# Optimization experiments

Hardware: AMD Instinct MI355X
Metric: run time of the kernel (lower is better)

## Reference

```python
import jax, jax.numpy as jnp
import numpy as np

GROUPS = 32
EPS = 1e-5
NUM_HEADS = 8


def group_norm(x, w, b):
    # x: (B, C, H, W)
    B, C, H, W = x.shape
    xg = x.reshape(B, GROUPS, C // GROUPS, H, W)
    mean = xg.mean(axis=(2, 3, 4), keepdims=True)
    var = xg.var(axis=(2, 3, 4), keepdims=True)
    xg = (xg - mean) * jax.lax.rsqrt(var + EPS)
    x = xg.reshape(B, C, H, W)
    return x * w[None, :, None, None] + b[None, :, None, None]


def setup_inputs() -> dict:
    key = jax.random.key(0)
    ks = jax.random.split(key, 4)
    B, C, H, W = 16, 512, 32, 32
    x = jax.random.normal(ks[0], (B, C, H, W), dtype=jnp.float32)
    gn_w = jnp.ones((C,), dtype=jnp.float32)
    gn_b = jnp.zeros((C,), dtype=jnp.float32)
    qkv_w = jax.random.normal(ks[1], (3 * C, C), dtype=jnp.float32) * 0.02  # 1x1 conv, no bias
    proj_w = jax.random.normal(ks[2], (C, C), dtype=jnp.float32) * 0.02     # 1x1 conv
    proj_b = jax.random.normal(ks[3], (C,), dtype=jnp.float32) * 0.02
    return {"x": x, "gn_w": gn_w, "gn_b": gn_b, "qkv_w": qkv_w,
            "proj_w": proj_w, "proj_b": proj_b}


def reference(x, gn_w, gn_b, qkv_w, proj_w, proj_b):
    B, C, H, W = x.shape
    heads = NUM_HEADS
    head_dim = C // heads
    HW = H * W
    scale = 1.0 / (head_dim ** 0.5)

    x = group_norm(x, gn_w, gn_b)  # residual uses the NORMED x, matching source

    qkv = jnp.einsum('bchw,oc->bohw', x, qkv_w)                     # (B, 3C, H, W)
    qkv = qkv.reshape(B, 3, heads, head_dim, HW)
    q, k, v = qkv[:, 0], qkv[:, 1], qkv[:, 2]                       # (B, heads, head_dim, HW)

    # Replicate the source's exact permute(0,2,3,1)+reshape (scrambles semantics, but faithful)
    def to_bmh(t):
        return jnp.transpose(t, (0, 2, 3, 1)).reshape(B * heads, HW, head_dim)
    q, k, v = to_bmh(q), to_bmh(k), to_bmh(v)

    attn = jax.nn.softmax(jnp.einsum('bnd,bmd->bnm', q, k) * scale, axis=-1)  # (B*heads, HW, HW)
    h = jnp.einsum('bnm,bmd->bnd', attn, v)                                   # (B*heads, HW, head_dim)

    h = h.reshape(B, heads, H, W, head_dim)
    h = jnp.transpose(h, (0, 1, 4, 2, 3)).reshape(B, C, H, W)

    out = jnp.einsum('bchw,oc->bohw', h, proj_w) + proj_b[None, :, None, None]
    return out + x
```

## Files before the change

### kernel.cpp

```cpp
#include <hip/hip_runtime.h>
#include <stdint.h>

typedef unsigned short u16;
typedef short bfrag __attribute__((ext_vector_type(8)));
typedef float ffrag __attribute__((ext_vector_type(4)));
typedef u16 us4 __attribute__((ext_vector_type(4)));
typedef uint32_t u32x4 __attribute__((ext_vector_type(4)));

#define HW 1024
#define C_DIM 512
#define O3 1536
#define BATCH 16

__device__ __forceinline__ u16 f2bf(float f) {
    uint32_t u = __builtin_bit_cast(uint32_t, f);
    u += 0x7FFFu + ((u >> 16) & 1u);
    return (u16)(u >> 16);
}
__device__ __forceinline__ float bf2f(u16 v) {
    return __builtin_bit_cast(float, (uint32_t)v << 16);
}
__device__ __forceinline__ float fexp2(float x) { return __builtin_amdgcn_exp2f(x); }
__device__ __forceinline__ void async16(const u16* src, u16* ldsDst) {
    __builtin_amdgcn_global_load_lds(
        (const __attribute__((address_space(1))) uint32_t*)src,
        (__attribute__((address_space(3))) uint32_t*)ldsDst, 16, 0, 0);
}

__global__ __launch_bounds__(256) void cvt2_kernel(const float* __restrict__ a, u16* __restrict__ da, int n4a,
                                                   const float* __restrict__ b, u16* __restrict__ db, int n4b) {
    int i = blockIdx.x * 256 + threadIdx.x;
    if (i < n4a) {
        float4 v = ((const float4*)a)[i];
        us4 o = { f2bf(v.x), f2bf(v.y), f2bf(v.z), f2bf(v.w) };
        ((us4*)da)[i] = o;
    } else {
        int j = i - n4a;
        if (j < n4b) {
            float4 v = ((const float4*)b)[j];
            us4 o = { f2bf(v.x), f2bf(v.y), f2bf(v.z), f2bf(v.w) };
            ((us4*)db)[j] = o;
        }
    }
}

__global__ __launch_bounds__(256) void groupnorm_kernel(
    const float* __restrict__ x, const float* __restrict__ gw, const float* __restrict__ gb,
    u16* __restrict__ xg, u16* __restrict__ xgt)
{
    __shared__ u16 tile[16 * 1032];
    __shared__ float red[8];
    const int tid = threadIdx.x;
    const int batch = blockIdx.x >> 5, g = blockIdx.x & 31;
    const float* xp = x + ((size_t)batch * C_DIM + g * 16) * HW;

    float s = 0.f, ss = 0.f;
#pragma unroll
    for (int it = 0; it < 16; ++it) {
        int i4 = it * 256 + tid;
        float4 v = ((const float4*)xp)[i4];
        int ci = i4 >> 8;
        int hw = (i4 & 255) * 4;
        s += v.x + v.y + v.z + v.w;
        ss += v.x * v.x + v.y * v.y + v.z * v.z + v.w * v.w;
        us4 u = { f2bf(v.x), f2bf(v.y), f2bf(v.z), f2bf(v.w) };
        *(us4*)&tile[ci * 1032 + hw] = u;
    }
#pragma unroll
    for (int m = 1; m <= 32; m <<= 1) { s += __shfl_xor(s, m, 64); ss += __shfl_xor(ss, m, 64); }
    if ((tid & 63) == 0) { red[tid >> 6] = s; red[4 + (tid >> 6)] = ss; }
    __syncthreads();
    float S = red[0] + red[1] + red[2] + red[3];
    float SS = red[4] + red[5] + red[6] + red[7];
    const float mean = S * (1.f / 16384.f);
    const float istd = rsqrtf(SS * (1.f / 16384.f) - mean * mean + 1e-5f);

    u16* xgp = xg + ((size_t)batch * C_DIM + g * 16) * HW;
#pragma unroll
    for (int it = 0; it < 16; ++it) {
        int i4 = it * 256 + tid;
        int ci = i4 >> 8;
        int hw = (i4 & 255) * 4;
        us4 u = *(us4*)&tile[ci * 1032 + hw];
        float sc = gw[g * 16 + ci] * istd;
        float bi = gb[g * 16 + ci] - mean * sc;
        us4 o = { f2bf(bf2f(u[0]) * sc + bi), f2bf(bf2f(u[1]) * sc + bi),
                  f2bf(bf2f(u[2]) * sc + bi), f2bf(bf2f(u[3]) * sc + bi) };
        *(us4*)&xgp[(size_t)ci * HW + hw] = o;
    }
    u16* xtp = xgt + (size_t)batch * HW * C_DIM + g * 16;
#pragma unroll
    for (int it = 0; it < 16; ++it) {
        int hw = (tid >> 2) + it * 64;
        int c0 = (tid & 3) * 4;
        us4 o;
#pragma unroll
        for (int k2 = 0; k2 < 4; ++k2) {
            int ci = c0 + k2;
            float sc = gw[g * 16 + ci] * istd;
            float bi = gb[g * 16 + ci] - mean * sc;
            o[k2] = f2bf(bf2f(tile[ci * 1032 + hw]) * sc + bi);
        }
        *(us4*)&xtp[(size_t)hw * C_DIM + c0] = o;
    }
}

__global__ __launch_bounds__(256, 2) void qkv_gemm_kernel(
    const u16* __restrict__ A, const u16* __restrict__ B, u16* __restrict__ Out,
    u16* __restrict__ vtout)
{
    __shared__ __align__(16) u16 smem[36864];
    const int tid = threadIdx.x;
    const int l = tid & 63, w = tid >> 6;
    const int swz = (blockIdx.x & 7) * 96 + (blockIdx.x >> 3);
    const int batch = swz / 48, t = swz % 48;
    const int tm = t / 12, tn = t % 12;
    A += (size_t)batch * (HW * C_DIM) + (size_t)tm * 256 * 512;
    B += (size_t)tn * 128 * 512;

    auto stageA = [&](u16* lds, int kt) {
#pragma unroll
        for (int i = 0; i < 4; ++i) {
            int L = i * 256 + tid;
            int row = L >> 2, cs = L & 3;
            int c = cs ^ ((row & 3) ^ ((row >> 2) & 3));
            async16(A + (size_t)row * 512 + kt * 32 + c * 8,
                    lds + (size_t)(i * 256 + (tid & 192)) * 8);
        }
    };
    auto stageB = [&](u16* lds, int kt) {
#pragma unroll
        for (int i = 0; i < 2; ++i) {
            int L = i * 256 + tid;
            int row = L >> 2, cs = L & 3;
            int c = cs ^ ((row & 3) ^ ((row >> 2) & 3));
            async16(B + (size_t)row * 512 + kt * 32 + c * 8,
                    lds + (size_t)(i * 256 + (tid & 192)) * 8);
        }
    };

    ffrag acc[8][4] = {};
    stageA(smem, 0);        stageB(smem + 24576, 0);
    stageA(smem + 8192, 1); stageB(smem + 28672, 1);
    const int wm = (w >> 1) * 128, wn = (w & 1) * 64;
#pragma unroll
    for (int kt = 0; kt < 16; ++kt) {
        const int cur = kt % 3;
        if (kt < 15) asm volatile("s_waitcnt vmcnt(6)" ::: "memory");
        else         asm volatile("s_waitcnt vmcnt(0)" ::: "memory");
        __builtin_amdgcn_s_barrier();
        __builtin_amdgcn_sched_barrier(0);
        if (kt < 14) {
            int nxt = (kt + 2) % 3;
            stageA(smem + nxt * 8192, kt + 2);
            stageB(smem + 24576 + nxt * 4096, kt + 2);
        }
        const u16* As = smem + cur * 8192;
        const u16* Bs = smem + 24576 + cur * 4096;
        bfrag a[8], bb[4];
#pragma unroll
        for (int j = 0; j < 4; ++j) {
            int col = wn + j * 16 + (l & 15);
            int ch2 = (l >> 4) ^ ((col & 3) ^ ((col >> 2) & 3));
            bb[j] = *(const bfrag*)&Bs[col * 32 + ch2 * 8];
        }
#pragma unroll
        for (int i = 0; i < 8; ++i) {
            int row = wm + i * 16 + (l & 15);
            int ch = (l >> 4) ^ ((row & 3) ^ ((row >> 2) & 3));
            a[i] = *(const bfrag*)&As[row * 32 + ch * 8];
        }
        __builtin_amdgcn_s_setprio(1);
#pragma unroll
        for (int i = 0; i < 8; ++i)
#pragma unroll
            for (int j = 0; j < 4; ++j)
                acc[i][j] = __builtin_amdgcn_mfma_f32_16x16x32_bf16(a[i], bb[j], acc[i][j], 0, 0, 0);
        __builtin_amdgcn_s_setprio(0);
    }
    __syncthreads();
    const int rbase = tm * 256 + wm + ((l >> 4) << 2);
    const int cbase = tn * 128 + wn + (l & 15);
    if (tn < 8) {
        u16* outp = Out + (size_t)batch * (HW * O3);
#pragma unroll
        for (int i = 0; i < 8; ++i)
#pragma unroll
            for (int j = 0; j < 4; ++j)
#pragma unroll
                for (int r = 0; r < 4; ++r)
                    outp[(size_t)(rbase + i * 16 + r) * O3 + cbase + j * 16] = f2bf(acc[i][j][r]);
    } else {
        u16* vb = vtout + (size_t)batch * 8 * 64 * HW;
        const int hd0 = tn * 128 - 1024;
#pragma unroll
        for (int i = 0; i < 8; ++i)
#pragma unroll
            for (int j = 0; j < 4; ++j) {
                int hd_l = wn + (l & 15) + j * 16;
                int m_l = wm + i * 16 + ((l >> 4) << 2);
                int s_l = (m_l & ~31) | ((m_l & 12) << 1) | ((m_l & 16) >> 2) | (m_l & 3);
                int c4 = s_l >> 2;
                int c4s = c4 ^ (hd_l & 63);
                us4 pk = { f2bf(acc[i][j][0]), f2bf(acc[i][j][1]),
                           f2bf(acc[i][j][2]), f2bf(acc[i][j][3]) };
                *(us4*)&smem[hd_l * 256 + c4s * 4] = pk;
            }
        __syncthreads();
#pragma unroll
        for (int it = 0; it < 32; ++it) {
            int f4 = it * 256 + tid;
            int hd_l = f4 >> 6, c4 = f4 & 63;
            int c4s = c4 ^ (hd_l & 63);
            us4 v = *(const us4*)&smem[hd_l * 256 + c4s * 4];
            *(us4*)&vb[(size_t)(hd0 + hd_l) * HW + tm * 256 + c4 * 4] = v;
        }
    }
}

__global__ __launch_bounds__(256) void proj_gemm_kernel(
    const u16* __restrict__ A, const u16* __restrict__ B, float* __restrict__ Out,
    const float* __restrict__ bias, const u16* __restrict__ resid)
{
    __shared__ __align__(16) u16 smem[24576];
    const int tid = threadIdx.x;
    const int l = tid & 63, w = tid >> 6;
    const int swz = (blockIdx.x & 7) * 64 + (blockIdx.x >> 3);
    const int batch = swz / 32, t = swz % 32;
    const int tm = t / 8, tn = t % 8;
    A += (size_t)tm * 128 * 512;
    B += (size_t)batch * (HW * C_DIM) + (size_t)tn * 128 * 512;

    auto stage = [&](const u16* gbase, u16* lds, int kt) {
#pragma unroll
        for (int i = 0; i < 2; ++i) {
            int L = i * 256 + tid;
            int row = L >> 2, cs = L & 3;
            int c = cs ^ ((row & 3) ^ ((row >> 2) & 3));
            async16(gbase + (size_t)row * 512 + kt * 32 + c * 8,
                    lds + (size_t)(i * 256 + (tid & 192)) * 8);
        }
    };

    ffrag acc[4][4] = {};
    stage(A, smem, 0);        stage(B, smem + 12288, 0);
    stage(A, smem + 4096, 1); stage(B, smem + 16384, 1);
    const int wr = (w >> 1) * 64, wc = (w & 1) * 64;
#pragma unroll
    for (int kt = 0; kt < 16; ++kt) {
        const int cur = kt % 3;
        if (kt < 15) asm volatile("s_waitcnt vmcnt(4)" ::: "memory");
        else         asm volatile("s_waitcnt vmcnt(0)" ::: "memory");
        __builtin_amdgcn_s_barrier();
        __builtin_amdgcn_sched_barrier(0);
        if (kt < 14) {
            int nxt = (kt + 2) % 3;
            stage(A, smem + nxt * 4096, kt + 2);
            stage(B, smem + 12288 + nxt * 4096, kt + 2);
        }
        const u16* As = smem + cur * 4096;
        const u16* Bs = smem + 12288 + cur * 4096;
        bfrag a[4], bb[4];
#pragma unroll
        for (int i = 0; i < 4; ++i) {
            int row = wr + i * 16 + (l & 15);
            int ch = (l >> 4) ^ ((row & 3) ^ ((row >> 2) & 3));
            a[i] = *(const bfrag*)&As[row * 32 + ch * 8];
            int col = wc + i * 16 + (l & 15);
            int ch2 = (l >> 4) ^ ((col & 3) ^ ((col >> 2) & 3));
            bb[i] = *(const bfrag*)&Bs[col * 32 + ch2 * 8];
        }
        __builtin_amdgcn_s_setprio(1);
#pragma unroll
        for (int i = 0; i < 4; ++i)
#pragma unroll
            for (int j = 0; j < 4; ++j)
                acc[i][j] = __builtin_amdgcn_mfma_f32_16x16x32_bf16(a[i], bb[j], acc[i][j], 0, 0, 0);
        __builtin_amdgcn_s_setprio(0);
    }
    const int rbase = tm * 128 + wr + ((l >> 4) << 2);
    const int cbase = tn * 128 + wc + (l & 15);
    float* outp = Out + (size_t)batch * (C_DIM * HW);
    const u16* rp = resid + (size_t)batch * (C_DIM * HW);
#pragma unroll
    for (int i = 0; i < 4; ++i)
#pragma unroll
        for (int j = 0; j < 4; ++j)
#pragma unroll
            for (int r = 0; r < 4; ++r) {
                int rr = rbase + i * 16 + r, cc = cbase + j * 16;
                outp[(size_t)rr * HW + cc] =
                    acc[i][j][r] + bias[rr] + bf2f(rp[(size_t)rr * HW + cc]);
            }
}

__global__ __launch_bounds__(512, 4) void attn_kernel(const u16* __restrict__ qkvt,
                                                      const u16* __restrict__ vt,
                                                      u16* __restrict__ ht)
{
    __shared__ __align__(16) u16 KVs[6 * 4096];
    const int tid = threadIdx.x, l = tid & 63, w = tid >> 6, g = l >> 4;
    const int swz = ((blockIdx.x & 7) << 6) + (blockIdx.x >> 3);
    const int nt = swz & 3, h = (swz >> 2) & 7, batch = swz >> 5;
    const u16* Qb = qkvt + (size_t)batch * HW * O3 + h * 64;
    const u16* Kb = Qb + 512;
    const u16* Vtb = vt + (size_t)(batch * 8 + h) * 64 * HW;
    const int n0 = nt * 256 + w * 32;
    const float cexp = 0.125f * 1.44269504f;

    bfrag qf[2][2];
#pragma unroll
    for (int ni = 0; ni < 2; ++ni)
#pragma unroll
        for (int kc = 0; kc < 2; ++kc)
            qf[ni][kc] = *(const bfrag*)&Qb[(size_t)(n0 + ni * 16 + (l & 15)) * O3 + kc * 32 + g * 8];

    bfrag ones;
#pragma unroll
    for (int k = 0; k < 8; ++k) ones[k] = (short)0x3F80;

    auto stageK = [&](int ms, u16* lds) {
        int row = tid >> 3, c = (tid & 7) ^ (row & 7);
        async16(&Kb[(size_t)(ms * 64 + row) * O3 + c * 8], lds + (size_t)(tid & 448) * 8);
    };
    auto stageV = [&](int ms, u16* lds) {
        int row = tid >> 3, c = (tid & 7) ^ (row & 7);
        async16(&Vtb[(size_t)row * HW + ms * 64 + c * 8], lds + (size_t)(tid & 448) * 8);
    };

    ffrag hacc[2][4] = {};
    ffrag accl[2] = {};

    stageK(0, KVs);        stageV(0, KVs + 3 * 4096);
    stageK(1, KVs + 4096); stageV(1, KVs + 4 * 4096);

#pragma unroll
    for (int ms = 0; ms < 16; ++ms) {
        const int cur = ms % 3;
        const u16* Ksc = KVs + cur * 4096;
        const u16* Vsc = KVs + (3 + cur) * 4096;
        if (ms < 15) asm volatile("s_waitcnt vmcnt(2)" ::: "memory");
        else         asm volatile("s_waitcnt vmcnt(0)" ::: "memory");
        __builtin_amdgcn_s_barrier();
        __builtin_amdgcn_sched_barrier(0);
        if (ms < 14) {
            int nxt = (ms + 2) % 3;
            stageK(ms + 2, KVs + nxt * 4096);
            stageV(ms + 2, KVs + (3 + nxt) * 4096);
        }

        ffrag s[2][4] = {};
        __builtin_amdgcn_s_setprio(1);
#pragma unroll
        for (int mj = 0; mj < 4; ++mj)
#pragma unroll
            for (int kc = 0; kc < 2; ++kc) {
                int m = mj * 16 + (l & 15);
                int ch = (kc * 4 + g) ^ (m & 7);
                bfrag kf = *(const bfrag*)&Ksc[m * 64 + ch * 8];
#pragma unroll
                for (int ni = 0; ni < 2; ++ni)
                    s[ni][mj] = __builtin_amdgcn_mfma_f32_16x16x32_bf16(kf, qf[ni][kc], s[ni][mj], 0, 0, 0);
            }
        __builtin_amdgcn_s_setprio(0);

        u32x4 pk[2][2];
#pragma unroll
        for (int ni = 0; ni < 2; ++ni)
#pragma unroll
            for (int kc = 0; kc < 2; ++kc)
#pragma unroll
                for (int hh = 0; hh < 2; ++hh) {
                    int mj = kc * 2 + hh;
                    float p0 = fexp2(s[ni][mj][0] * cexp);
                    float p1 = fexp2(s[ni][mj][1] * cexp);
                    float p2 = fexp2(s[ni][mj][2] * cexp);
                    float p3 = fexp2(s[ni][mj][3] * cexp);
                    pk[ni][kc][hh * 2] = __builtin_amdgcn_perm(
                        __builtin_bit_cast(uint32_t, p1), __builtin_bit_cast(uint32_t, p0), 0x07060302u);
                    pk[ni][kc][hh * 2 + 1] = __builtin_amdgcn_perm(
                        __builtin_bit_cast(uint32_t, p3), __builtin_bit_cast(uint32_t, p2), 0x07060302u);
                }

        __builtin_amdgcn_s_setprio(1);
#pragma unroll
        for (int kc = 0; kc < 2; ++kc) {
            bfrag pf0 = __builtin_bit_cast(bfrag, pk[0][kc]);
            bfrag pf1 = __builtin_bit_cast(bfrag, pk[1][kc]);
            accl[0] = __builtin_amdgcn_mfma_f32_16x16x32_bf16(pf0, ones, accl[0], 0, 0, 0);
            accl[1] = __builtin_amdgcn_mfma_f32_16x16x32_bf16(pf1, ones, accl[1], 0, 0, 0);
#pragma unroll
            for (int dj = 0; dj < 4; ++dj) {
                int d = dj * 16 + (l & 15);
                int ch = (kc * 4 + g) ^ (d & 7);
                bfrag vf = *(const bfrag*)&Vsc[d * 64 + ch * 8];
                hacc[0][dj] = __builtin_amdgcn_mfma_f32_16x16x32_bf16(pf0, vf, hacc[0][dj], 0, 0, 0);
                hacc[1][dj] = __builtin_amdgcn_mfma_f32_16x16x32_bf16(pf1, vf, hacc[1][dj], 0, 0, 0);
            }
        }
        __builtin_amdgcn_s_setprio(0);
    }

    u16* hp = ht + (size_t)batch * HW * C_DIM + h * 64;
#pragma unroll
    for (int ni = 0; ni < 2; ++ni) {
        float linv[4];
#pragma unroll
        for (int r = 0; r < 4; ++r) linv[r] = __builtin_amdgcn_rcpf(accl[ni][r]);
#pragma unroll
        for (int dj = 0; dj < 4; ++dj)
#pragma unroll
            for (int r = 0; r < 4; ++r) {
                int n = n0 + ni * 16 + g * 4 + r;
                int d = dj * 16 + (l & 15);
                hp[(size_t)n * C_DIM + d] = f2bf(hacc[ni][dj][r] * linv[r]);
            }
    }
}

extern "C" void kernel_launch(void* const* d_in, const int* in_sizes, int n_in,
                              void* d_out, int out_size, void* d_ws, size_t ws_size,
                              hipStream_t stream)
{
    const float* x = (const float*)d_in[0];
    const float* gw = (const float*)d_in[1];
    const float* gb = (const float*)d_in[2];
    const float* qkvw = (const float*)d_in[3];
    const float* projw = (const float*)d_in[4];
    const float* projb = (const float*)d_in[5];
    float* out = (float*)d_out;
    char* ws = (char*)d_ws;
    u16* xg    = (u16*)(ws);
    u16* xgt   = (u16*)(ws + 16777216);
    u16* qkvt  = (u16*)(ws + 33554432);
    u16* vt    = (u16*)(ws + 83886080);
    u16* qkvwb = (u16*)(ws + 100663296);
    u16* projwb= (u16*)(ws + 102236160);
    u16* ht    = xgt;

    cvt2_kernel<<<1024, 256, 0, stream>>>(qkvw, qkvwb, 196608, projw, projwb, 65536);
    groupnorm_kernel<<<512, 256, 0, stream>>>(x, gw, gb, xg, xgt);
    qkv_gemm_kernel<<<768, 256, 0, stream>>>(xgt, qkvwb, qkvt, vt);
    attn_kernel<<<512, 512, 0, stream>>>(qkvt, vt, ht);
    proj_gemm_kernel<<<512, 256, 0, stream>>>(projwb, ht, out, projb, xg);
}
```

Baseline: 111.1 us.

## Merge weight conversion into groupnorm and drop duplicate normalized-x layout

Folds the weight fp32-to-bf16 conversion into the groupnorm launch as extra blocks, removing one kernel launch. It also stops writing the channel-major normalized copy; the projection epilogue now reads the residual from the transposed normalized buffer with a 4-element vector load. The attention output is moved to its own buffer so the transposed normalized tensor stays alive for the residual. This saves a 16 MB write, but the residual reads in proj are now strided across C for each output column.

After: 105.9 us. 4.7% less time.

```diff
diff --git a/kernel.cpp b/kernel.cpp
--- a/kernel.cpp
+++ b/kernel.cpp
@@ -27,30 +27,29 @@
         (__attribute__((address_space(3))) uint32_t*)ldsDst, 16, 0, 0);
 }
 
-__global__ __launch_bounds__(256) void cvt2_kernel(const float* __restrict__ a, u16* __restrict__ da, int n4a,
-                                                   const float* __restrict__ b, u16* __restrict__ db, int n4b) {
-    int i = blockIdx.x * 256 + threadIdx.x;
-    if (i < n4a) {
-        float4 v = ((const float4*)a)[i];
-        us4 o = { f2bf(v.x), f2bf(v.y), f2bf(v.z), f2bf(v.w) };
-        ((us4*)da)[i] = o;
-    } else {
-        int j = i - n4a;
-        if (j < n4b) {
-            float4 v = ((const float4*)b)[j];
-            us4 o = { f2bf(v.x), f2bf(v.y), f2bf(v.z), f2bf(v.w) };
-            ((us4*)db)[j] = o;
-        }
-    }
-}
-
-__global__ __launch_bounds__(256) void groupnorm_kernel(
+__global__ __launch_bounds__(256) void gn_cvt_kernel(
     const float* __restrict__ x, const float* __restrict__ gw, const float* __restrict__ gb,
-    u16* __restrict__ xg, u16* __restrict__ xgt)
+    u16* __restrict__ xgt,
+    const float* __restrict__ qkvw, u16* __restrict__ qkvwb,
+    const float* __restrict__ projw, u16* __restrict__ projwb)
 {
     __shared__ u16 tile[16 * 1032];
     __shared__ float red[8];
     const int tid = threadIdx.x;
+    if (blockIdx.x >= 512) {
+        int i = (blockIdx.x - 512) * 256 + tid;
+        if (i < 196608) {
+            float4 v = ((const float4*)qkvw)[i];
+            us4 o = { f2bf(v.x), f2bf(v.y), f2bf(v.z), f2bf(v.w) };
+            ((us4*)qkvwb)[i] = o;
+        } else {
+            int j = i - 196608;
+            float4 v = ((const float4*)projw)[j];
+            us4 o = { f2bf(v.x), f2bf(v.y), f2bf(v.z), f2bf(v.w) };
+            ((us4*)projwb)[j] = o;
+        }
+        return;
+    }
     const int batch = blockIdx.x >> 5, g = blockIdx.x & 31;
     const float* xp = x + ((size_t)batch * C_DIM + g * 16) * HW;
 
@@ -75,19 +74,6 @@
     const float mean = S * (1.f / 16384.f);
     const float istd = rsqrtf(SS * (1.f / 16384.f) - mean * mean + 1e-5f);
 
-    u16* xgp = xg + ((size_t)batch * C_DIM + g * 16) * HW;
-#pragma unroll
-    for (int it = 0; it < 16; ++it) {
-        int i4 = it * 256 + tid;
-        int ci = i4 >> 8;
-        int hw = (i4 & 255) * 4;
-        us4 u = *(us4*)&tile[ci * 1032 + hw];
-        float sc = gw[g * 16 + ci] * istd;
-        float bi = gb[g * 16 + ci] - mean * sc;
-        us4 o = { f2bf(bf2f(u[0]) * sc + bi), f2bf(bf2f(u[1]) * sc + bi),
-                  f2bf(bf2f(u[2]) * sc + bi), f2bf(bf2f(u[3]) * sc + bi) };
-        *(us4*)&xgp[(size_t)ci * HW + hw] = o;
-    }
     u16* xtp = xgt + (size_t)batch * HW * C_DIM + g * 16;
 #pragma unroll
     for (int it = 0; it < 16; ++it) {
@@ -220,7 +206,7 @@
 
 __global__ __launch_bounds__(256) void proj_gemm_kernel(
     const u16* __restrict__ A, const u16* __restrict__ B, float* __restrict__ Out,
-    const float* __restrict__ bias, const u16* __restrict__ resid)
+    const float* __restrict__ bias, const u16* __restrict__ residT)
 {
     __shared__ __align__(16) u16 smem[24576];
     const int tid = threadIdx.x;
@@ -281,17 +267,19 @@
     const int rbase = tm * 128 + wr + ((l >> 4) << 2);
     const int cbase = tn * 128 + wc + (l & 15);
     float* outp = Out + (size_t)batch * (C_DIM * HW);
-    const u16* rp = resid + (size_t)batch * (C_DIM * HW);
+    const u16* rt = residT + (size_t)batch * (HW * C_DIM);
 #pragma unroll
     for (int i = 0; i < 4; ++i)
 #pragma unroll
-        for (int j = 0; j < 4; ++j)
+        for (int j = 0; j < 4; ++j) {
+            int cc = cbase + j * 16;
+            us4 rv = *(const us4*)&rt[(size_t)cc * C_DIM + rbase + i * 16];
 #pragma unroll
             for (int r = 0; r < 4; ++r) {
-                int rr = rbase + i * 16 + r, cc = cbase + j * 16;
-                outp[(size_t)rr * HW + cc] =
-                    acc[i][j][r] + bias[rr] + bf2f(rp[(size_t)rr * HW + cc]);
+                int rr = rbase + i * 16 + r;
+                outp[(size_t)rr * HW + cc] = acc[i][j][r] + bias[rr] + bf2f(rv[r]);
             }
+        }
 }
 
 __global__ __launch_bounds__(512, 4) void attn_kernel(const u16* __restrict__ qkvt,
@@ -430,17 +418,15 @@
     const float* projb = (const float*)d_in[5];
     float* out = (float*)d_out;
     char* ws = (char*)d_ws;
-    u16* xg    = (u16*)(ws);
+    u16* ht    = (u16*)(ws);
     u16* xgt   = (u16*)(ws + 16777216);
     u16* qkvt  = (u16*)(ws + 33554432);
     u16* vt    = (u16*)(ws + 83886080);
     u16* qkvwb = (u16*)(ws + 100663296);
     u16* projwb= (u16*)(ws + 102236160);
-    u16* ht    = xgt;
-
-    cvt2_kernel<<<1024, 256, 0, stream>>>(qkvw, qkvwb, 196608, projw, projwb, 65536);
-    groupnorm_kernel<<<512, 256, 0, stream>>>(x, gw, gb, xg, xgt);
+
+    gn_cvt_kernel<<<1536, 256, 0, stream>>>(x, gw, gb, xgt, qkvw, qkvwb, projw, projwb);
     qkv_gemm_kernel<<<768, 256, 0, stream>>>(xgt, qkvwb, qkvt, vt);
     attn_kernel<<<512, 512, 0, stream>>>(qkvt, vt, ht);
-    proj_gemm_kernel<<<512, 256, 0, stream>>>(projwb, ht, out, projb, xg);
-}
+    proj_gemm_kernel<<<512, 256, 0, stream>>>(projwb, ht, out, projb, xgt);
+}
```
